# Optimization experiments

Measured on AMD Instinct MI355X. Metric: run time of the kernel, lower is better.

## Reference

```python
import jax, jax.numpy as jnp
from jax import lax
import numpy as np

IMG_W = 384; IMG_H = 384; FEAT = 24; RF = 16
RATIOS = (0.5, 1.0, 2.0); SCALES = (8.0, 16.0, 32.0)
K = 9                      # len(RATIOS) * len(SCALES)
N = FEAT * FEAT * K        # 5184 anchors/proposals
MID = 24; CIN = 512
NMS_THRESH = 0.7; MIN_SIZE = 16.0


def _make_anchors():
    # Faithful port of RPN._get_anchors (vectorized over the grid).
    area = float(RF * RF)
    base = []
    for r in RATIOS:
        cols = np.round(np.sqrt(area / r)); rows = np.round(cols * r)
        x0 = 0.5 * RF - 0.5 * (cols - 1); x1 = 0.5 * RF + 0.5 * (cols - 1)
        y0 = 0.5 * RF - 0.5 * (rows - 1); y1 = 0.5 * RF + 0.5 * (rows - 1)
        aw = x1 - x0 + 1; ah = y1 - y0 + 1
        acx = x0 + 0.5 * (aw - 1); acy = y0 + 0.5 * (ah - 1)
        for s in SCALES:
            nx0 = acx - 0.5 * (aw * s - 1.0); nx1 = acx + 0.5 * (aw * s - 1.0)
            ny0 = acy - 0.5 * (ah * s - 1.0); ny1 = acy + 0.5 * (ah * s - 1.0)
            w = nx1 - nx0 + 1; h = ny1 - ny0 + 1
            base.append([nx0 + 0.5 * (w - 1), ny0 + 0.5 * (h - 1), w, h])
    base = np.asarray(base, np.float32)  # (K,4) as (cx, cy, w, h)
    ii, jj = np.meshgrid(np.arange(FEAT), np.arange(FEAT), indexing='ij')
    g = np.broadcast_to(base, (FEAT, FEAT, K, 4)).copy()  # (H, W, K, 4)
    g[..., 0] += (jj * RF)[:, :, None]
    g[..., 1] += (ii * RF)[:, :, None]
    a = g.reshape(-1, 4)  # matches permute(1,2,0).reshape(-1,4) ordering
    ax0 = a[:, 0] - 0.5 * (a[:, 2] - 1.0); ay0 = a[:, 1] - 0.5 * (a[:, 3] - 1.0)
    ax1 = a[:, 2] + ax0 - 1.0; ay1 = a[:, 3] + ay0 - 1.0
    valid = (ax0 >= 0) & (ay0 >= 0) & (ax1 < IMG_W) & (ay1 < IMG_H)
    return jnp.asarray(a, jnp.float32), jnp.asarray(valid)


def setup_inputs() -> dict:
    key = jax.random.key(0)
    ks = jax.random.split(key, 6)
    anchors, valid_mask = _make_anchors()
    return {
        'x': jax.random.normal(ks[0], (1, CIN, FEAT, FEAT), jnp.float32),
        'labels_class': jax.random.randint(ks[1], (N,), 0, 21, jnp.int32),
        'W_rpn': jax.random.normal(ks[2], (MID, CIN, 3, 3), jnp.float32) * 0.02,
        'b_rpn': jnp.zeros((MID,), jnp.float32),
        'W_cls': jax.random.normal(ks[3], (2 * K, MID), jnp.float32) * 0.05,
        'b_cls': jnp.zeros((2 * K,), jnp.float32),
        'W_reg': jax.random.normal(ks[4], (4 * K, MID), jnp.float32) * 0.01,
        'b_reg': jnp.zeros((4 * K,), jnp.float32),
        'anchors': anchors,
        'valid_mask': valid_mask,
    }


def _forward(x, W_rpn, b_rpn, W_cls, b_cls, W_reg, b_reg, anchors, valid_mask, labels_class):
    # 3x3 conv + relu, then 1x1 cls/reg heads
    h = jax.nn.relu(
        lax.conv_general_dilated(x, W_rpn, (1, 1), ((1, 1), (1, 1)),
                                 dimension_numbers=('NCHW', 'OIHW', 'NCHW'))
        + b_rpn[None, :, None, None])
    cls_out = (jnp.einsum('nchw,oc->nohw', h, W_cls) + b_cls[None, :, None, None])[0]
    cls_out = cls_out.transpose(1, 2, 0).reshape(-1, 2)   # [N,2]
    reg_out = (jnp.einsum('nchw,oc->nohw', h, W_reg) + b_reg[None, :, None, None])[0]
    reg_out = reg_out.transpose(1, 2, 0).reshape(-1, 4)   # [N,4]

    # anchors -> proposals (cx, cy, w, h); computed for all anchors, validity masked below
    ax, ay, aw, ah = anchors[:, 0], anchors[:, 1], anchors[:, 2], anchors[:, 3]
    tx, ty, tw, th = reg_out[:, 0], reg_out[:, 1], reg_out[:, 2], reg_out[:, 3]
    px = ax + aw * tx; py = ay + ah * ty
    pw = aw * jnp.exp(tw); ph = ah * jnp.exp(th)
    proposals = jnp.stack((px, py, pw, ph), axis=1)

    # offset2bbox + clip_boxes
    x0 = px - 0.5 * (pw - 1.0); y0 = py - 0.5 * (ph - 1.0)
    x1 = pw + x0 - 1.0; y1 = ph + y0 - 1.0
    x0 = jnp.clip(x0, 0.0, IMG_W - 1.0); x1 = jnp.clip(x1, 0.0, IMG_W - 1.0)
    y0 = jnp.clip(y0, 0.0, IMG_H - 1.0); y1 = jnp.clip(y1, 0.0, IMG_H - 1.0)
    ws = x1 - x0 + 1.0; hs = y1 - y0 + 1.0

    probs = jax.nn.softmax(cls_out, axis=1)[:, 1]
    validity = valid_mask & (ws >= MIN_SIZE) & (hs >= MIN_SIZE)

    # greedy NMS (padded/masked: invalid boxes get score -1 and are never kept)
    scores = jnp.where(validity, probs, -1.0)
    order = jnp.argsort(-scores)
    bx0, by0, bx1, by1 = x0[order], y0[order], x1[order], y1[order]
    v_sorted = validity[order]
    areas = ws[order] * hs[order]
    iw = jnp.clip(jnp.minimum(bx1[:, None], bx1[None, :]) - jnp.maximum(bx0[:, None], bx0[None, :]) + 1.0, 0.0)
    ih = jnp.clip(jnp.minimum(by1[:, None], by1[None, :]) - jnp.maximum(by0[:, None], by0[None, :]) + 1.0, 0.0)
    inter = iw * ih
    iou = inter / (areas[:, None] + areas[None, :] - inter)  # [N,N]
    idxs = jnp.arange(N)

    def body(sup, xs):
        i, row, v = xs
        keep_i = v & jnp.logical_not(sup[i])
        sup = jnp.where(keep_i, sup | ((row > NMS_THRESH) & (idxs > i)), sup)
        return sup, keep_i

    _, keep_sorted = lax.scan(body, jnp.zeros((N,), bool), (idxs, iou, v_sorted))
    keep = jnp.zeros((N,), bool).at[order].set(keep_sorted)
    keepf = keep.astype(probs.dtype)

    # bbox2offset of kept boxes (padded: suppressed rows zeroed)
    filtered = jnp.stack((x0 + 0.5 * (ws - 1.0), y0 + 0.5 * (hs - 1.0), ws, hs), axis=1) * keepf[:, None]
    probs_kept = probs * keepf
    labels_kept = jnp.where(keep, labels_class, 0)
    return proposals, cls_out, filtered, probs_kept, labels_kept, keep


def reference(x, labels_class, W_rpn, b_rpn, W_cls, b_cls, W_reg, b_reg, anchors, valid_mask):
    return _forward(x, W_rpn, b_rpn, W_cls, b_cls, W_reg, b_reg, anchors, valid_mask, labels_class)
```

## Files before the change

kernel.cpp:

```cpp
#include <hip/hip_runtime.h>
#include <hip/hip_bf16.h>
#include <math.h>

#define NANC   5184
#define NPOS   576
#define CIN    512
#define MIDC   24
#define KANC   9
#define IMGW   384.0f
#define IMGM1  383.0f
#define MINSZ  16.0f
#define THRESH 0.7f

#define OFF_PROP 0
#define OFF_CLS  20736
#define OFF_FILT 31104
#define OFF_PK   51840
#define OFF_LBL  57024
#define OFF_KEEP 62208

#define MCAP 896
#define GCAP 14
#define TOTW (64 * (GCAP*(GCAP+1)/2))

#define WS_XT    0
#define WS_WT    1179648
#define WS_BOX   1622016
#define WS_PROB  1953792
#define WS_KEYS  2036736
#define WS_SIDX  2044928
#define WS_SBOX  2049024
#define WS_MASK  2063360
#define WS_CNT   2117120

__global__ __launch_bounds__(256) void k_prep(const float* __restrict__ x,
                                              const float* __restrict__ W,
                                              float* __restrict__ xt,
                                              float* __restrict__ Wt,
                                              unsigned* cnt) {
    int tid = blockIdx.x * 256 + threadIdx.x;
    if (tid == 0) *cnt = 0;
    const int TOT = CIN * NPOS + MIDC * CIN * 9;
    for (int idx = tid; idx < TOT; idx += gridDim.x * 256) {
        if (idx < CIN * NPOS) {
            int pos = idx >> 9, ic = idx & 511;
            xt[idx] = x[ic * NPOS + pos];
        } else {
            int k = idx - CIN * NPOS;
            int ic = k & 511; int t = k >> 9;
            int oc = t / 9, kk = t % 9;
            Wt[k] = W[(oc * CIN + ic) * 9 + kk];
        }
    }
}

__global__ __launch_bounds__(256) void k_main(
        const float* __restrict__ xt, const float* __restrict__ Wt,
        const float* __restrict__ brpn,
        const float* __restrict__ Wc, const float* __restrict__ bc,
        const float* __restrict__ Wr, const float* __restrict__ br,
        const float* __restrict__ anchors,
        float* __restrict__ out, float4* __restrict__ boxes,
        float* __restrict__ probs, unsigned long long* __restrict__ vkeys,
        unsigned* __restrict__ cnt) {
    const int tid = threadIdx.x;
    const int y = blockIdx.x / 6;
    const int xb = (blockIdx.x % 6) * 4;

    float acc[24][4];
    #pragma unroll
    for (int oc = 0; oc < 24; ++oc)
        #pragma unroll
        for (int p = 0; p < 4; ++p) acc[oc][p] = 0.f;

    for (int half = 0; half < 2; ++half) {
        const int ic = tid + half * 256;
        float xw[3][6];
        #pragma unroll
        for (int r = 0; r < 3; ++r) {
            int yy = y - 1 + r;
            #pragma unroll
            for (int c = 0; c < 6; ++c) {
                int xx = xb - 1 + c;
                bool in = (yy >= 0) & (yy < 24) & (xx >= 0) & (xx < 24);
                xw[r][c] = in ? xt[(yy * 24 + xx) * CIN + ic] : 0.f;
            }
        }
        const float* wp = Wt + ic;
        #pragma unroll
        for (int oc = 0; oc < 24; ++oc) {
            #pragma unroll
            for (int kk = 0; kk < 9; ++kk) {
                const int r = kk / 3, c = kk % 3;
                float wv = wp[(oc * 9 + kk) * CIN];
                #pragma unroll
                for (int p = 0; p < 4; ++p)
                    acc[oc][p] += wv * xw[r][c + p];
            }
        }
    }
    #pragma unroll
    for (int oc = 0; oc < 24; ++oc)
        #pragma unroll
        for (int p = 0; p < 4; ++p) {
            float v = acc[oc][p];
            #pragma unroll
            for (int m = 1; m < 64; m <<= 1) v += __shfl_xor(v, m, 64);
            acc[oc][p] = v;
        }

    __shared__ float red[4][96];
    __shared__ float h_ld[4 * 24];
    __shared__ float cls_ld[4 * 18];
    __shared__ float reg_ld[4 * 36];
    const int wave = tid >> 6, lane = tid & 63;
    if (lane == 0) {
        #pragma unroll
        for (int oc = 0; oc < 24; ++oc)
            #pragma unroll
            for (int p = 0; p < 4; ++p) red[wave][oc * 4 + p] = acc[oc][p];
    }
    __syncthreads();
    if (tid < 96) {
        float s = red[0][tid] + red[1][tid] + red[2][tid] + red[3][tid];
        int oc = tid >> 2, p = tid & 3;
        h_ld[p * 24 + oc] = fmaxf(s + brpn[oc], 0.f);
    }
    __syncthreads();
    if (tid < 216) {
        int p = tid / 54, o = tid % 54;
        const float* hv = h_ld + p * 24;
        if (o < 18) {
            float s = bc[o];
            const float* w = Wc + o * 24;
            #pragma unroll
            for (int c = 0; c < 24; ++c) s += w[c] * hv[c];
            cls_ld[p * 18 + o] = s;
            out[OFF_CLS + (y * 24 + xb + p) * 18 + o] = s;
        } else {
            int o2 = o - 18;
            float s = br[o2];
            const float* w = Wr + o2 * 24;
            #pragma unroll
            for (int c = 0; c < 24; ++c) s += w[c] * hv[c];
            reg_ld[p * 36 + o2] = s;
        }
    }
    __syncthreads();
    if (tid < 36) {
        #pragma clang fp contract(off)
        int p = tid / 9, k = tid % 9;
        int n = (y * 24 + xb + p) * 9 + k;
        float ax = anchors[4 * n], ay = anchors[4 * n + 1];
        float aw = anchors[4 * n + 2], ah = anchors[4 * n + 3];
        float tx = reg_ld[p * 36 + 4 * k],     ty = reg_ld[p * 36 + 4 * k + 1];
        float tw = reg_ld[p * 36 + 4 * k + 2], th = reg_ld[p * 36 + 4 * k + 3];
        float px = ax + aw * tx, py = ay + ah * ty;
        float pw = aw * expf(tw), ph = ah * expf(th);
        out[OFF_PROP + 4 * n]     = px;
        out[OFF_PROP + 4 * n + 1] = py;
        out[OFF_PROP + 4 * n + 2] = pw;
        out[OFF_PROP + 4 * n + 3] = ph;
        float gx0 = ax - 0.5f * (aw - 1.f);
        float gy0 = ay - 0.5f * (ah - 1.f);
        float gx1 = aw + gx0 - 1.f;
        float gy1 = ah + gy0 - 1.f;
        bool geo_ok = (gx0 >= 0.f) & (gy0 >= 0.f) & (gx1 < IMGW) & (gy1 < IMGW);
        float x0 = px - 0.5f * (pw - 1.f);
        float y0 = py - 0.5f * (ph - 1.f);
        float x1 = pw + x0 - 1.f;
        float y1 = ph + y0 - 1.f;
        x0 = fminf(fmaxf(x0, 0.f), IMGM1);
        x1 = fminf(fmaxf(x1, 0.f), IMGM1);
        y0 = fminf(fmaxf(y0, 0.f), IMGM1);
        y1 = fminf(fmaxf(y1, 0.f), IMGM1);
        float wsb = x1 - x0 + 1.f, hsb = y1 - y0 + 1.f;
        float c0 = cls_ld[p * 18 + 2 * k], c1 = cls_ld[p * 18 + 2 * k + 1];
        float mx = fmaxf(c0, c1);
        float e0 = expf(c0 - mx), e1 = expf(c1 - mx);
        float pr = e1 / (e0 + e1);
        boxes[n] = make_float4(x0, y0, x1, y1);
        probs[n] = pr;
        bool valid = geo_ok && (wsb >= MINSZ) && (hsb >= MINSZ);
        if (valid) {
            unsigned pos = atomicAdd(cnt, 1u);
            unsigned u = __float_as_uint(pr);
            unsigned enc = u ^ ((u >> 31) ? 0xFFFFFFFFu : 0x80000000u);
            vkeys[pos] = ((unsigned long long)(~enc) << 32) | (unsigned)n;
        }
    }
}

__global__ __launch_bounds__(512) void k_sort(const unsigned long long* __restrict__ vkeys,
                                              const unsigned* __restrict__ cnt,
                                              int* __restrict__ sidx,
                                              float4* __restrict__ sbox,
                                              const float4* __restrict__ boxes) {
    __shared__ unsigned long long keys[1024];
    const int t = threadIdx.x;
    unsigned Mc = *cnt; unsigned M = Mc < (unsigned)MCAP ? Mc : (unsigned)MCAP;
    for (int i = t; i < 1024; i += 512) keys[i] = (i < (int)M) ? vkeys[i] : ~0ULL;
    __syncthreads();
    for (int k = 2; k <= 1024; k <<= 1) {
        for (int j = k >> 1; j > 0; j >>= 1) {
            int lo = t & (j - 1);
            int i = ((t ^ lo) << 1) | lo;
            int pa = i | j;
            bool up = (i & k) == 0;
            unsigned long long a = keys[i], b = keys[pa];
            if ((a > b) == up) { keys[i] = b; keys[pa] = a; }
            __syncthreads();
        }
    }
    for (int i = t; i < (int)M; i += 512) {
        int n = (int)(keys[i] & 0xFFFFFFFFu);
        sidx[i] = n;
        sbox[i] = boxes[n];
    }
}

__global__ __launch_bounds__(256) void k_mask(const float4* __restrict__ sbox,
                                              const unsigned* __restrict__ cnt,
                                              unsigned long long* __restrict__ mask) {
    __shared__ float4 sb[MCAP];
    const int t = threadIdx.x;
    for (int i = t; i < MCAP; i += 256) sb[i] = sbox[i];
    __syncthreads();
    unsigned Mc = *cnt; unsigned M = Mc < (unsigned)MCAP ? Mc : (unsigned)MCAP;
    int widx = blockIdx.x * 256 + t;
    if (widx >= TOTW) return;
    int g = 0, base = 0;
    while (g < GCAP - 1) {
        int nb = base + 64 * (GCAP - g);
        if (widx < nb) break;
        base = nb; ++g;
    }
    int rem = widx - base;
    int r = rem / (GCAP - g);
    int gw = g + rem % (GCAP - g);
    int i = g * 64 + r;
    if (i >= (int)M) return;
    {
        #pragma clang fp contract(off)
        float4 bi = sb[i];
        float ai = (bi.z - bi.x + 1.f) * (bi.w - bi.y + 1.f);
        unsigned long long w = 0;
        #pragma unroll 4
        for (int b = 0; b < 64; ++b) {
            int j = gw * 64 + b;
            if (j > i) {
                float4 bj = sb[j];
                float iw = fminf(bi.z, bj.z) - fmaxf(bi.x, bj.x) + 1.f;
                float ih = fminf(bi.w, bj.w) - fmaxf(bi.y, bj.y) + 1.f;
                iw = fmaxf(iw, 0.f); ih = fmaxf(ih, 0.f);
                float inter = iw * ih;
                float aj = (bj.z - bj.x + 1.f) * (bj.w - bj.y + 1.f);
                float iou = inter / (ai + aj - inter);
                if (iou > THRESH) w |= 1ULL << b;
            }
        }
        mask[widx] = w;
    }
}

__global__ __launch_bounds__(1024) void k_nms(const unsigned long long* __restrict__ mask_g,
                                              const int* __restrict__ sidx_g,
                                              const unsigned* __restrict__ cnt,
                                              const float4* __restrict__ boxes,
                                              const float* __restrict__ probs,
                                              const int* __restrict__ labels,
                                              float* __restrict__ out) {
    __shared__ unsigned long long mk[TOTW];
    __shared__ int sidx[MCAP];
    __shared__ unsigned long long keepm[81];
    __shared__ unsigned long long keeps[GCAP];
    __shared__ unsigned long long suppw[GCAP];
    const int t = threadIdx.x;
    unsigned Mc = *cnt; unsigned M = Mc < (unsigned)MCAP ? Mc : (unsigned)MCAP;
    for (int i = t; i < TOTW; i += 1024) mk[i] = mask_g[i];
    if (t < MCAP) sidx[t] = sidx_g[t];
    if (t < 81) keepm[t] = 0;
    if (t < GCAP) { keeps[t] = 0; suppw[t] = 0; }
    __syncthreads();
    const int wid = t >> 6, lane = t & 63;
    const int ngroups = (int)((M + 63) >> 6);
    for (int g = 0; g < ngroups; ++g) {
        const int rowstride = GCAP - g;
        const int base_g = 64 * (GCAP * g - (g * (g - 1)) / 2);
        int nbits = (int)M - g * 64; if (nbits > 64) nbits = 64;
        unsigned long long vmaskbits = (nbits < 64) ? ((1ULL << nbits) - 1ULL) : ~0ULL;
        if (wid == 0) {
            unsigned long long diag = mk[base_g + lane * rowstride];
            unsigned dlo = (unsigned)diag, dhi = (unsigned)(diag >> 32);
            unsigned long long supp = suppw[g];
            unsigned long long nz = __ballot(diag != 0ULL) & vmaskbits;
            while (nz) {
                int r = __ffsll(nz) - 1;
                nz &= nz - 1;
                if (!((supp >> r) & 1ULL)) {
                    unsigned rlo = (unsigned)__builtin_amdgcn_readlane((int)dlo, r);
                    unsigned rhi = (unsigned)__builtin_amdgcn_readlane((int)dhi, r);
                    supp |= ((unsigned long long)rhi << 32) | rlo;
                }
            }
            if (lane == 0) keeps[g] = ~supp & vmaskbits;
        }
        __syncthreads();
        if (wid > g && wid < GCAP) {
            unsigned long long kw = keeps[g];
            unsigned long long v = ((kw >> lane) & 1ULL)
                ? mk[base_g + lane * rowstride + (wid - g)] : 0ULL;
            unsigned vlo = (unsigned)v, vhi = (unsigned)(v >> 32);
            #pragma unroll
            for (int m = 1; m < 64; m <<= 1) {
                vlo |= __shfl_xor(vlo, m, 64);
                vhi |= __shfl_xor(vhi, m, 64);
            }
            if (lane == 0)
                suppw[wid] |= ((unsigned long long)vhi << 32) | vlo;
        }
        __syncthreads();
    }
    if (t < (int)M) {
        if ((keeps[t >> 6] >> (t & 63)) & 1ULL) {
            int n = sidx[t];
            atomicOr(&keepm[n >> 6], 1ULL << (n & 63));
        }
    }
    __syncthreads();
    for (int n = t; n < NANC; n += 1024) {
        unsigned long long kb = (keepm[n >> 6] >> (n & 63)) & 1ULL;
        float kf = kb ? 1.f : 0.f;
        float4 b = boxes[n];
        float wsb = b.z - b.x + 1.f, hsb = b.w - b.y + 1.f;
        out[OFF_FILT + 4 * n]     = (b.x + 0.5f * (wsb - 1.f)) * kf;
        out[OFF_FILT + 4 * n + 1] = (b.y + 0.5f * (hsb - 1.f)) * kf;
        out[OFF_FILT + 4 * n + 2] = wsb * kf;
        out[OFF_FILT + 4 * n + 3] = hsb * kf;
        out[OFF_PK + n]  = probs[n] * kf;
        out[OFF_LBL + n] = kb ? (float)labels[n] : 0.f;
        out[OFF_KEEP + n] = kf;
    }
}

extern "C" void kernel_launch(void* const* d_in, const int* in_sizes, int n_in,
                              void* d_out, int out_size, void* d_ws, size_t ws_size,
                              hipStream_t stream) {
    const float* x        = (const float*)d_in[0];
    const int*   labels   = (const int*)d_in[1];
    const float* Wrpn     = (const float*)d_in[2];
    const float* brpn     = (const float*)d_in[3];
    const float* Wcls     = (const float*)d_in[4];
    const float* bcls     = (const float*)d_in[5];
    const float* Wreg     = (const float*)d_in[6];
    const float* breg     = (const float*)d_in[7];
    const float* anchors  = (const float*)d_in[8];
    float* out = (float*)d_out;
    char* ws = (char*)d_ws;

    float*  xt    = (float*)(ws + WS_XT);
    float*  Wt    = (float*)(ws + WS_WT);
    float4* boxes = (float4*)(ws + WS_BOX);
    float*  probs = (float*)(ws + WS_PROB);
    unsigned long long* vkeys = (unsigned long long*)(ws + WS_KEYS);
    int*    sidx  = (int*)(ws + WS_SIDX);
    float4* sbox  = (float4*)(ws + WS_SBOX);
    unsigned long long* mask = (unsigned long long*)(ws + WS_MASK);
    unsigned* cnt = (unsigned*)(ws + WS_CNT);

    k_prep<<<1584, 256, 0, stream>>>(x, Wrpn, xt, Wt, cnt);
    k_main<<<144, 256, 0, stream>>>(xt, Wt, brpn, Wcls, bcls, Wreg, breg,
                                    anchors, out, boxes, probs, vkeys, cnt);
    k_sort<<<1, 512, 0, stream>>>(vkeys, cnt, sidx, sbox, boxes);
    k_mask<<<27, 256, 0, stream>>>(sbox, cnt, mask);
    k_nms<<<1, 1024, 0, stream>>>(mask, sidx, cnt, boxes, probs, labels, out);
}
```

Measured before the change: 139.3 us.

## Drop transpose prep kernel, read x/W directly, replace bitonic sort with rank sort

Removes the k_prep transpose kernel. The conv kernel now reads x and W in their original layout, using 512 threads (one input channel each), and the counter is reset with hipMemsetAsync. The single-block bitonic sort is replaced by a multi-block rank sort, where each key counts how many keys are smaller, spread over GCAP blocks of 64 threads. The direct reads are strided per thread rather than coalesced, which trades memory efficiency for one fewer launch and no extra global round trip. The filtered-box output is also written as a float4.

```diff
diff --git a/kernel.cpp b/kernel.cpp
--- a/kernel.cpp
+++ b/kernel.cpp
@@ -23,8 +23,6 @@
 #define GCAP 14
 #define TOTW (64 * (GCAP*(GCAP+1)/2))
 
-#define WS_XT    0
-#define WS_WT    1179648
 #define WS_BOX   1622016
 #define WS_PROB  1953792
 #define WS_KEYS  2036736
@@ -33,29 +31,8 @@
 #define WS_MASK  2063360
 #define WS_CNT   2117120
 
-__global__ __launch_bounds__(256) void k_prep(const float* __restrict__ x,
-                                              const float* __restrict__ W,
-                                              float* __restrict__ xt,
-                                              float* __restrict__ Wt,
-                                              unsigned* cnt) {
-    int tid = blockIdx.x * 256 + threadIdx.x;
-    if (tid == 0) *cnt = 0;
-    const int TOT = CIN * NPOS + MIDC * CIN * 9;
-    for (int idx = tid; idx < TOT; idx += gridDim.x * 256) {
-        if (idx < CIN * NPOS) {
-            int pos = idx >> 9, ic = idx & 511;
-            xt[idx] = x[ic * NPOS + pos];
-        } else {
-            int k = idx - CIN * NPOS;
-            int ic = k & 511; int t = k >> 9;
-            int oc = t / 9, kk = t % 9;
-            Wt[k] = W[(oc * CIN + ic) * 9 + kk];
-        }
-    }
-}
-
-__global__ __launch_bounds__(256) void k_main(
-        const float* __restrict__ xt, const float* __restrict__ Wt,
+__global__ __launch_bounds__(512) void k_main(
+        const float* __restrict__ x, const float* __restrict__ W,
         const float* __restrict__ brpn,
         const float* __restrict__ Wc, const float* __restrict__ bc,
         const float* __restrict__ Wr, const float* __restrict__ br,
@@ -67,36 +44,35 @@
     const int y = blockIdx.x / 6;
     const int xb = (blockIdx.x % 6) * 4;
 
+    float xw[3][6];
+    const float* xc = x + tid * NPOS;
+    #pragma unroll
+    for (int r = 0; r < 3; ++r) {
+        int yy = y - 1 + r;
+        #pragma unroll
+        for (int c = 0; c < 6; ++c) {
+            int xx = xb - 1 + c;
+            bool in = (yy >= 0) & (yy < 24) & (xx >= 0) & (xx < 24);
+            xw[r][c] = in ? xc[yy * 24 + xx] : 0.f;
+        }
+    }
+
     float acc[24][4];
     #pragma unroll
     for (int oc = 0; oc < 24; ++oc)
         #pragma unroll
         for (int p = 0; p < 4; ++p) acc[oc][p] = 0.f;
 
-    for (int half = 0; half < 2; ++half) {
-        const int ic = tid + half * 256;
-        float xw[3][6];
-        #pragma unroll
-        for (int r = 0; r < 3; ++r) {
-            int yy = y - 1 + r;
-            #pragma unroll
-            for (int c = 0; c < 6; ++c) {
-                int xx = xb - 1 + c;
-                bool in = (yy >= 0) & (yy < 24) & (xx >= 0) & (xx < 24);
-                xw[r][c] = in ? xt[(yy * 24 + xx) * CIN + ic] : 0.f;
-            }
-        }
-        const float* wp = Wt + ic;
-        #pragma unroll
-        for (int oc = 0; oc < 24; ++oc) {
-            #pragma unroll
-            for (int kk = 0; kk < 9; ++kk) {
-                const int r = kk / 3, c = kk % 3;
-                float wv = wp[(oc * 9 + kk) * CIN];
-                #pragma unroll
-                for (int p = 0; p < 4; ++p)
-                    acc[oc][p] += wv * xw[r][c + p];
-            }
+    const float* wp = W + tid * 9;
+    #pragma unroll
+    for (int oc = 0; oc < 24; ++oc) {
+        #pragma unroll
+        for (int kk = 0; kk < 9; ++kk) {
+            const int r = kk / 3, c = kk % 3;
+            float wv = wp[oc * (CIN * 9) + kk];
+            #pragma unroll
+            for (int p = 0; p < 4; ++p)
+                acc[oc][p] += wv * xw[r][c + p];
         }
     }
     #pragma unroll
@@ -109,7 +85,7 @@
             acc[oc][p] = v;
         }
 
-    __shared__ float red[4][96];
+    __shared__ float red[8][96];
     __shared__ float h_ld[4 * 24];
     __shared__ float cls_ld[4 * 18];
     __shared__ float reg_ld[4 * 36];
@@ -122,7 +98,9 @@
     }
     __syncthreads();
     if (tid < 96) {
-        float s = red[0][tid] + red[1][tid] + red[2][tid] + red[3][tid];
+        float s = 0.f;
+        #pragma unroll
+        for (int w = 0; w < 8; ++w) s += red[w][tid];
         int oc = tid >> 2, p = tid & 3;
         h_ld[p * 24 + oc] = fmaxf(s + brpn[oc], 0.f);
     }
@@ -191,31 +169,25 @@
     }
 }
 
-__global__ __launch_bounds__(512) void k_sort(const unsigned long long* __restrict__ vkeys,
-                                              const unsigned* __restrict__ cnt,
-                                              int* __restrict__ sidx,
-                                              float4* __restrict__ sbox,
-                                              const float4* __restrict__ boxes) {
-    __shared__ unsigned long long keys[1024];
+__global__ __launch_bounds__(64) void k_rank(const unsigned long long* __restrict__ vkeys,
+                                             const unsigned* __restrict__ cnt,
+                                             int* __restrict__ sidx,
+                                             float4* __restrict__ sbox,
+                                             const float4* __restrict__ boxes) {
+    __shared__ unsigned long long keys[MCAP];
     const int t = threadIdx.x;
-    unsigned Mc = *cnt; unsigned M = Mc < (unsigned)MCAP ? Mc : (unsigned)MCAP;
-    for (int i = t; i < 1024; i += 512) keys[i] = (i < (int)M) ? vkeys[i] : ~0ULL;
-    __syncthreads();
-    for (int k = 2; k <= 1024; k <<= 1) {
-        for (int j = k >> 1; j > 0; j >>= 1) {
-            int lo = t & (j - 1);
-            int i = ((t ^ lo) << 1) | lo;
-            int pa = i | j;
-            bool up = (i & k) == 0;
-            unsigned long long a = keys[i], b = keys[pa];
-            if ((a > b) == up) { keys[i] = b; keys[pa] = a; }
-            __syncthreads();
-        }
-    }
-    for (int i = t; i < (int)M; i += 512) {
-        int n = (int)(keys[i] & 0xFFFFFFFFu);
-        sidx[i] = n;
-        sbox[i] = boxes[n];
+    unsigned Mc = *cnt; int M = (int)(Mc < (unsigned)MCAP ? Mc : (unsigned)MCAP);
+    for (int i = t; i < M; i += 64) keys[i] = vkeys[i];
+    __syncthreads();
+    int i = blockIdx.x * 64 + t;
+    if (i < M) {
+        unsigned long long ki = keys[i];
+        int r = 0;
+        #pragma unroll 4
+        for (int j = 0; j < M; ++j) r += (keys[j] < ki) ? 1 : 0;
+        int n = (int)(ki & 0xFFFFFFFFu);
+        sidx[r] = n;
+        sbox[r] = boxes[n];
     }
 }
 
@@ -333,10 +305,12 @@
         float kf = kb ? 1.f : 0.f;
         float4 b = boxes[n];
         float wsb = b.z - b.x + 1.f, hsb = b.w - b.y + 1.f;
-        out[OFF_FILT + 4 * n]     = (b.x + 0.5f * (wsb - 1.f)) * kf;
-        out[OFF_FILT + 4 * n + 1] = (b.y + 0.5f * (hsb - 1.f)) * kf;
-        out[OFF_FILT + 4 * n + 2] = wsb * kf;
-        out[OFF_FILT + 4 * n + 3] = hsb * kf;
+        float4 fo;
+        fo.x = (b.x + 0.5f * (wsb - 1.f)) * kf;
+        fo.y = (b.y + 0.5f * (hsb - 1.f)) * kf;
+        fo.z = wsb * kf;
+        fo.w = hsb * kf;
+        *reinterpret_cast<float4*>(out + OFF_FILT + 4 * n) = fo;
         out[OFF_PK + n]  = probs[n] * kf;
         out[OFF_LBL + n] = kb ? (float)labels[n] : 0.f;
         out[OFF_KEEP + n] = kf;
@@ -358,8 +332,6 @@
     float* out = (float*)d_out;
     char* ws = (char*)d_ws;
 
-    float*  xt    = (float*)(ws + WS_XT);
-    float*  Wt    = (float*)(ws + WS_WT);
     float4* boxes = (float4*)(ws + WS_BOX);
     float*  probs = (float*)(ws + WS_PROB);
     unsigned long long* vkeys = (unsigned long long*)(ws + WS_KEYS);
@@ -368,10 +340,10 @@
     unsigned long long* mask = (unsigned long long*)(ws + WS_MASK);
     unsigned* cnt = (unsigned*)(ws + WS_CNT);
 
-    k_prep<<<1584, 256, 0, stream>>>(x, Wrpn, xt, Wt, cnt);
-    k_main<<<144, 256, 0, stream>>>(xt, Wt, brpn, Wcls, bcls, Wreg, breg,
+    hipMemsetAsync(cnt, 0, 4, stream);
+    k_main<<<144, 512, 0, stream>>>(x, Wrpn, brpn, Wcls, bcls, Wreg, breg,
                                     anchors, out, boxes, probs, vkeys, cnt);
-    k_sort<<<1, 512, 0, stream>>>(vkeys, cnt, sidx, sbox, boxes);
+    k_rank<<<GCAP, 64, 0, stream>>>(vkeys, cnt, sidx, sbox, boxes);
     k_mask<<<27, 256, 0, stream>>>(sbox, cnt, mask);
     k_nms<<<1, 1024, 0, stream>>>(mask, sidx, cnt, boxes, probs, labels, out);
 }
```

Measured after the change: 149.6 us. 1.07x slower.

## Replace single-block bitonic sort with multi-block rank sort; vectorize filtered-box stores

Applied to the files above, without the earlier changes.

Replaces the one-block 1024-element bitonic sort, which needs 55 barrier-separated passes, with a rank sort spread over 14 blocks of 64 threads. Each thread counts how many keys are smaller than its own key and scatters to that rank; the keys are unique because the anchor index is packed into them. This trades O(M^2) total comparisons for no barriers and more parallel blocks. It also writes the four filtered-box outputs as one float4 store.

```diff
diff --git a/kernel.cpp b/kernel.cpp
--- a/kernel.cpp
+++ b/kernel.cpp
@@ -191,31 +191,25 @@
     }
 }
 
-__global__ __launch_bounds__(512) void k_sort(const unsigned long long* __restrict__ vkeys,
-                                              const unsigned* __restrict__ cnt,
-                                              int* __restrict__ sidx,
-                                              float4* __restrict__ sbox,
-                                              const float4* __restrict__ boxes) {
-    __shared__ unsigned long long keys[1024];
+__global__ __launch_bounds__(64) void k_rank(const unsigned long long* __restrict__ vkeys,
+                                             const unsigned* __restrict__ cnt,
+                                             int* __restrict__ sidx,
+                                             float4* __restrict__ sbox,
+                                             const float4* __restrict__ boxes) {
+    __shared__ unsigned long long keys[MCAP];
     const int t = threadIdx.x;
-    unsigned Mc = *cnt; unsigned M = Mc < (unsigned)MCAP ? Mc : (unsigned)MCAP;
-    for (int i = t; i < 1024; i += 512) keys[i] = (i < (int)M) ? vkeys[i] : ~0ULL;
-    __syncthreads();
-    for (int k = 2; k <= 1024; k <<= 1) {
-        for (int j = k >> 1; j > 0; j >>= 1) {
-            int lo = t & (j - 1);
-            int i = ((t ^ lo) << 1) | lo;
-            int pa = i | j;
-            bool up = (i & k) == 0;
-            unsigned long long a = keys[i], b = keys[pa];
-            if ((a > b) == up) { keys[i] = b; keys[pa] = a; }
-            __syncthreads();
-        }
-    }
-    for (int i = t; i < (int)M; i += 512) {
-        int n = (int)(keys[i] & 0xFFFFFFFFu);
-        sidx[i] = n;
-        sbox[i] = boxes[n];
+    unsigned Mc = *cnt; int M = (int)(Mc < (unsigned)MCAP ? Mc : (unsigned)MCAP);
+    for (int i = t; i < M; i += 64) keys[i] = vkeys[i];
+    __syncthreads();
+    int i = blockIdx.x * 64 + t;
+    if (i < M) {
+        unsigned long long ki = keys[i];
+        int r = 0;
+        #pragma unroll 4
+        for (int j = 0; j < M; ++j) r += (keys[j] < ki) ? 1 : 0;
+        int n = (int)(ki & 0xFFFFFFFFu);
+        sidx[r] = n;
+        sbox[r] = boxes[n];
     }
 }
 
@@ -333,10 +327,12 @@
         float kf = kb ? 1.f : 0.f;
         float4 b = boxes[n];
         float wsb = b.z - b.x + 1.f, hsb = b.w - b.y + 1.f;
-        out[OFF_FILT + 4 * n]     = (b.x + 0.5f * (wsb - 1.f)) * kf;
-        out[OFF_FILT + 4 * n + 1] = (b.y + 0.5f * (hsb - 1.f)) * kf;
-        out[OFF_FILT + 4 * n + 2] = wsb * kf;
-        out[OFF_FILT + 4 * n + 3] = hsb * kf;
+        float4 fo;
+        fo.x = (b.x + 0.5f * (wsb - 1.f)) * kf;
+        fo.y = (b.y + 0.5f * (hsb - 1.f)) * kf;
+        fo.z = wsb * kf;
+        fo.w = hsb * kf;
+        *reinterpret_cast<float4*>(out + OFF_FILT + 4 * n) = fo;
         out[OFF_PK + n]  = probs[n] * kf;
         out[OFF_LBL + n] = kb ? (float)labels[n] : 0.f;
         out[OFF_KEEP + n] = kf;
@@ -371,7 +367,7 @@
     k_prep<<<1584, 256, 0, stream>>>(x, Wrpn, xt, Wt, cnt);
     k_main<<<144, 256, 0, stream>>>(xt, Wt, brpn, Wcls, bcls, Wreg, breg,
                                     anchors, out, boxes, probs, vkeys, cnt);
-    k_sort<<<1, 512, 0, stream>>>(vkeys, cnt, sidx, sbox, boxes);
+    k_rank<<<GCAP, 64, 0, stream>>>(vkeys, cnt, sidx, sbox, boxes);
     k_mask<<<27, 256, 0, stream>>>(sbox, cnt, mask);
     k_nms<<<1, 1024, 0, stream>>>(mask, sidx, cnt, boxes, probs, labels, out);
 }
```

After: 149.6 us. +7.4%, slower.
